# Kernel tuning notes

Hardware: AMD Instinct MI355X
Metric: run time of the kernel (lower is better)

## Reference

```python
import jax, jax.numpy as jnp
import numpy as np

N = 100000
E = 1600000
D = 128
BN_EPS = 1e-5


def setup_inputs() -> dict:
    key = jax.random.key(0)
    ks = jax.random.split(key, 12)
    s = 1.0 / np.sqrt(D)
    x = jax.random.normal(ks[0], (N, D), dtype=jnp.float32)
    edge_index = jax.random.randint(ks[1], (2, E), 0, N, dtype=jnp.int64)
    # Linear weights stored as [in, out] (i.e. torch W.T)
    w1a = jax.random.uniform(ks[2], (D, D), jnp.float32, -s, s)
    b1a = jax.random.uniform(ks[3], (D,), jnp.float32, -s, s)
    w1b = jax.random.uniform(ks[4], (D, D), jnp.float32, -s, s)
    b1b = jax.random.uniform(ks[5], (D,), jnp.float32, -s, s)
    gamma2 = jnp.ones((D,), jnp.float32)
    beta2 = jnp.zeros((D,), jnp.float32)
    w2a = jax.random.uniform(ks[6], (D, D), jnp.float32, -s, s)
    b2a = jax.random.uniform(ks[7], (D,), jnp.float32, -s, s)
    w2b = jax.random.uniform(ks[8], (D, D), jnp.float32, -s, s)
    b2b = jax.random.uniform(ks[9], (D,), jnp.float32, -s, s)
    return dict(x=x, edge_index=edge_index, w1a=w1a, b1a=b1a, w1b=w1b, b1b=b1b,
                gamma2=gamma2, beta2=beta2, w2a=w2a, b2a=b2a, w2b=w2b, b2b=b2b)


def _gin_conv(h, src, dst, wa, ba, wb, bb):
    # GINConv (eps=0): nn(sum_{j in N(i)} h_j + h_i), then 2-layer MLP
    agg = jax.ops.segment_sum(h[src], dst, num_segments=h.shape[0])
    z = agg + h
    z = jax.nn.relu(z @ wa + ba)
    return z @ wb + bb


def reference(x, edge_index, w1a, b1a, w1b, b1b, gamma2, beta2, w2a, b2a, w2b, b2b):
    src, dst = edge_index[0], edge_index[1]
    h = _gin_conv(x, src, dst, w1a, b1a, w1b, b1b)
    h = jax.nn.relu(h)
    # BatchNorm1d in training mode: batch mean / biased variance
    mean = jnp.mean(h, axis=0)
    var = jnp.mean((h - mean) ** 2, axis=0)
    h = (h - mean) * jax.lax.rsqrt(var + BN_EPS) * gamma2 + beta2
    return _gin_conv(h, src, dst, w2a, b2a, w2b, b2b)
```

## Files before the change

kernel.cpp:

```cpp
#include <hip/hip_runtime.h>

#define NNODES 100000
#define NEDGES 1600000
#define DIM 128
#define BN_EPS 1e-5f
#define NBUCK 1024
#define NB_USED ((NNODES + 127) / 128)

typedef unsigned int uint;
typedef unsigned short ushort_t;
using bhalf8  = __attribute__((ext_vector_type(8))) short;
using u16x8   = __attribute__((ext_vector_type(8))) unsigned short;
using f32x4_t = __attribute__((ext_vector_type(4))) float;

__device__ __forceinline__ float bf2f(uint u16) {
    return __uint_as_float(u16 << 16);
}
__device__ __forceinline__ uint pack2_bf16rn(float a, float b) {
    uint ua = __float_as_uint(a); ua += 0x7FFFu + ((ua >> 16) & 1u);
    uint ub = __float_as_uint(b); ub += 0x7FFFu + ((ub >> 16) & 1u);
    return __builtin_amdgcn_perm(ub, ua, 0x07060302u);
}

__device__ __forceinline__ int edge_src(const int* ei, int fl, int e) {
    return fl ? ei[2 * e] : ei[e];
}
__device__ __forceinline__ int edge_dst(const int* ei, int fl, int e) {
    return fl ? ei[2 * (NEDGES + e)] : ei[NEDGES + e];
}

__global__ __launch_bounds__(256) void k_setup(const int* __restrict__ ei,
                                               float* __restrict__ stats,
                                               int* __restrict__ flag,
                                               int* __restrict__ bcnt) {
    int t = threadIdx.x;
    stats[t] = 0.0f;
    ((int4*)bcnt)[t] = make_int4(0, 0, 0, 0);
    if (t == 0) {
        int orr = 0;
        for (int i = 1; i < 128; i += 2) orr |= ei[i];
        *flag = (orr == 0) ? 1 : 0;
    }
}

__global__ __launch_bounds__(256) void k_bcount(const int* __restrict__ ei,
                                                const int* __restrict__ flag,
                                                int* __restrict__ bcnt) {
    __shared__ int h[NBUCK];
    int t = threadIdx.x;
    for (int i = t; i < NBUCK; i += 256) h[i] = 0;
    __syncthreads();
    int fl = *flag;
    int per = (NEDGES + gridDim.x - 1) / gridDim.x;
    int e0 = blockIdx.x * per;
    int e1 = min(e0 + per, NEDGES);
    for (int e = e0 + t; e < e1; e += 256)
        atomicAdd(&h[edge_dst(ei, fl, e) >> 7], 1);
    __syncthreads();
    for (int i = t; i < NBUCK; i += 256)
        if (h[i]) atomicAdd(&bcnt[i], h[i]);
}

__global__ __launch_bounds__(256) void k_bscan(const int* __restrict__ bcnt,
                                               int* __restrict__ bstart,
                                               int* __restrict__ bcur) {
    __shared__ int wtot[4];
    int t = threadIdx.x, lane = t & 63, w = t >> 6;
    int4 v = ((const int4*)bcnt)[t];
    int s = v.x + v.y + v.z + v.w;
    int sc = s;
#pragma unroll
    for (int d = 1; d < 64; d <<= 1) {
        int n = __shfl_up(sc, d, 64);
        if (lane >= d) sc += n;
    }
    if (lane == 63) wtot[w] = sc;
    __syncthreads();
    int woff = 0;
    for (int i = 0; i < w; ++i) woff += wtot[i];
    int excl = woff + sc - s;
    int o0 = excl, o1 = o0 + v.x, o2 = o1 + v.y, o3 = o2 + v.z;
    bstart[t * 4]     = o0;  bcur[t * 4]     = o0;
    bstart[t * 4 + 1] = o1;  bcur[t * 4 + 1] = o1;
    bstart[t * 4 + 2] = o2;  bcur[t * 4 + 2] = o2;
    bstart[t * 4 + 3] = o3;  bcur[t * 4 + 3] = o3;
    if (t == 255) bstart[NBUCK] = o3 + v.w;
}

__global__ __launch_bounds__(256) void k_bpair(const int* __restrict__ ei,
                                               const int* __restrict__ flag,
                                               int* __restrict__ bcur,
                                               int* __restrict__ pairs) {
    __shared__ int h[NBUCK];
    __shared__ int base[NBUCK];
    int t = threadIdx.x;
    for (int i = t; i < NBUCK; i += 256) h[i] = 0;
    __syncthreads();
    int fl = *flag;
    int per = (NEDGES + gridDim.x - 1) / gridDim.x;
    int e0 = blockIdx.x * per;
    int e1 = min(e0 + per, NEDGES);
    for (int e = e0 + t; e < e1; e += 256)
        atomicAdd(&h[edge_dst(ei, fl, e) >> 7], 1);
    __syncthreads();
    for (int i = t; i < NBUCK; i += 256) {
        int c = h[i];
        base[i] = c ? atomicAdd(&bcur[i], c) : 0;
    }
    __syncthreads();
    for (int i = t; i < NBUCK; i += 256) h[i] = 0;
    __syncthreads();
    for (int e = e0 + t; e < e1; e += 256) {
        int s = edge_src(ei, fl, e);
        int d = edge_dst(ei, fl, e);
        int b = d >> 7;
        int pos = atomicAdd(&h[b], 1);
        pairs[base[b] + pos] = (s << 7) | (d & 127);
    }
}

__global__ __launch_bounds__(256) void k_bsort(const int* __restrict__ pairs,
                                               const int* __restrict__ bstart,
                                               int* __restrict__ C,
                                               int* __restrict__ ssrc) {
    __shared__ int cnt[128];
    __shared__ int off[128];
    int b = blockIdx.x;
    int t = threadIdx.x, lane = t & 63, w = t >> 6;
    int s = bstart[b], e = bstart[b + 1];
    if (t < 128) cnt[t] = 0;
    __syncthreads();
    for (int i = s + t; i < e; i += 256)
        atomicAdd(&cnt[pairs[i] & 127], 1);
    __syncthreads();
    if (w == 0) {
        int c0 = cnt[lane], c1 = cnt[64 + lane];
        int s0 = c0, s1 = c1;
#pragma unroll
        for (int d = 1; d < 64; d <<= 1) {
            int n0 = __shfl_up(s0, d, 64);
            int n1 = __shfl_up(s1, d, 64);
            if (lane >= d) { s0 += n0; s1 += n1; }
        }
        int tot0 = __shfl(s0, 63, 64);
        off[lane]      = s0 - c0;
        off[64 + lane] = tot0 + s1 - c1;
    }
    __syncthreads();
    if (t < 128) {
        int row = b * 128 + t;
        if (row < NNODES) C[row] = s + off[t] + cnt[t];
    }
    __syncthreads();
    for (int i = s + t; i < e; i += 256) {
        int p = pairs[i];
        int pos = atomicAdd(&off[p & 127], 1);
        ssrc[s + pos] = p >> 7;
    }
}

__global__ __launch_bounds__(256) void k_wprep(const float* __restrict__ w0,
                                               const float* __restrict__ w1,
                                               const float* __restrict__ w2,
                                               const float* __restrict__ w3,
                                               ushort_t* __restrict__ ob) {
    const float* w = (blockIdx.x == 0) ? w0 : (blockIdx.x == 1) ? w1
                   : (blockIdx.x == 2) ? w2 : w3;
    ushort_t* oh = ob + (size_t)blockIdx.x * 16384;
    for (int i = threadIdx.x; i < 16384; i += 256) {
        int k = i >> 7, n = i & 127;
        uint u = __float_as_uint(w[i]);
        u += 0x7FFFu + ((u >> 16) & 1u);
        oh[n * 128 + k] = (ushort_t)(u >> 16);
    }
}

__global__ __launch_bounds__(256) void k_xconv(const float* __restrict__ X,
                                               ushort_t* __restrict__ Xb) {
    size_t i = ((size_t)blockIdx.x * 256 + threadIdx.x) * 8;
    float4 a = *(const float4*)(X + i);
    float4 b = *(const float4*)(X + i + 4);
    union { uint4 q; u16x8 v; } o;
    o.q.x = pack2_bf16rn(a.x, a.y);
    o.q.y = pack2_bf16rn(a.z, a.w);
    o.q.z = pack2_bf16rn(b.x, b.y);
    o.q.w = pack2_bf16rn(b.z, b.w);
    *(u16x8*)(Xb + i) = o.v;
}

__device__ __forceinline__ void split8(const float4& f0, const float4& f1,
                                       bhalf8& h, bhalf8& l) {
    uint u[8] = { __float_as_uint(f0.x), __float_as_uint(f0.y),
                  __float_as_uint(f0.z), __float_as_uint(f0.w),
                  __float_as_uint(f1.x), __float_as_uint(f1.y),
                  __float_as_uint(f1.z), __float_as_uint(f1.w) };
    float fv[8] = { f0.x, f0.y, f0.z, f0.w, f1.x, f1.y, f1.z, f1.w };
    uint lu[8];
#pragma unroll
    for (int i = 0; i < 8; ++i) {
        float hf = __uint_as_float(u[i] & 0xffff0000u);
        lu[i] = __float_as_uint(fv[i] - hf);
    }
    union { uint4 q; bhalf8 s; } H, L;
    H.q.x = __builtin_amdgcn_perm(u[1], u[0], 0x07060302u);
    H.q.y = __builtin_amdgcn_perm(u[3], u[2], 0x07060302u);
    H.q.z = __builtin_amdgcn_perm(u[5], u[4], 0x07060302u);
    H.q.w = __builtin_amdgcn_perm(u[7], u[6], 0x07060302u);
    L.q.x = __builtin_amdgcn_perm(lu[1], lu[0], 0x07060302u);
    L.q.y = __builtin_amdgcn_perm(lu[3], lu[2], 0x07060302u);
    L.q.z = __builtin_amdgcn_perm(lu[5], lu[4], 0x07060302u);
    L.q.w = __builtin_amdgcn_perm(lu[7], lu[6], 0x07060302u);
    h = H.s; l = L.s;
}

template <bool BN, bool SELF_F32>
__global__ __launch_bounds__(256) void k_agg(const ushort_t* __restrict__ Xb,
                                             const float* __restrict__ Xf,
                                             float* __restrict__ Z,
                                             const int* __restrict__ ends,
                                             const int* __restrict__ ssrc,
                                             const float* __restrict__ scale,
                                             const float* __restrict__ shift) {
    int t = threadIdx.x;
    int g = t >> 4;
    int l = t & 15;
    int row = blockIdx.x * 16 + g;
    int c8 = l * 8;
    int start = (row == 0) ? 0 : ends[row - 1];
    int end = ends[row];

    float acc[8];
    if (SELF_F32) {
        float4 a0 = *(const float4*)(Xf + (size_t)row * DIM + c8);
        float4 a1 = *(const float4*)(Xf + (size_t)row * DIM + c8 + 4);
        acc[0] = a0.x; acc[1] = a0.y; acc[2] = a0.z; acc[3] = a0.w;
        acc[4] = a1.x; acc[5] = a1.y; acc[6] = a1.z; acc[7] = a1.w;
    } else {
        union { u16x8 v; uint u[4]; } sv;
        sv.v = *(const u16x8*)(Xb + (size_t)row * DIM + c8);
#pragma unroll
        for (int i = 0; i < 4; ++i) {
            acc[2 * i]     = bf2f(sv.u[i] << 16 >> 16);
            acc[2 * i + 1] = __uint_as_float(sv.u[i] & 0xffff0000u);
        }
    }

    int e = start;
    for (; e + 7 < end; e += 8) {
        union { u16x8 v; uint u[4]; } nv[8];
#pragma unroll
        for (int i = 0; i < 8; ++i) {
            int s0 = ssrc[e + i];
            nv[i].v = *(const u16x8*)(Xb + (size_t)s0 * DIM + c8);
        }
#pragma unroll
        for (int i = 0; i < 8; ++i) {
#pragma unroll
            for (int j = 0; j < 4; ++j) {
                acc[2 * j]     += bf2f(nv[i].u[j] & 0xffffu);
                acc[2 * j + 1] += __uint_as_float(nv[i].u[j] & 0xffff0000u);
            }
        }
    }
    for (; e < end; ++e) {
        int s0 = ssrc[e];
        union { u16x8 v; uint u[4]; } nv;
        nv.v = *(const u16x8*)(Xb + (size_t)s0 * DIM + c8);
#pragma unroll
        for (int j = 0; j < 4; ++j) {
            acc[2 * j]     += bf2f(nv.u[j] & 0xffffu);
            acc[2 * j + 1] += __uint_as_float(nv.u[j] & 0xffff0000u);
        }
    }

    if (BN) {
        float4 sc0 = *(const float4*)(scale + c8);
        float4 sc1 = *(const float4*)(scale + c8 + 4);
        float4 sh0 = *(const float4*)(shift + c8);
        float4 sh1 = *(const float4*)(shift + c8 + 4);
        float cnt = (float)(end - start + 1);
        acc[0] = fmaf(acc[0], sc0.x, cnt * sh0.x);
        acc[1] = fmaf(acc[1], sc0.y, cnt * sh0.y);
        acc[2] = fmaf(acc[2], sc0.z, cnt * sh0.z);
        acc[3] = fmaf(acc[3], sc0.w, cnt * sh0.w);
        acc[4] = fmaf(acc[4], sc1.x, cnt * sh1.x);
        acc[5] = fmaf(acc[5], sc1.y, cnt * sh1.y);
        acc[6] = fmaf(acc[6], sc1.z, cnt * sh1.z);
        acc[7] = fmaf(acc[7], sc1.w, cnt * sh1.w);
    }
    float* zp = Z + (size_t)row * DIM + c8;
    *(float4*)zp       = make_float4(acc[0], acc[1], acc[2], acc[3]);
    *(float4*)(zp + 4) = make_float4(acc[4], acc[5], acc[6], acc[7]);
}

__global__ void k_bn(float* stats, const float* __restrict__ gamma,
                     const float* __restrict__ beta) {
    int c = threadIdx.x;
    float s  = stats[c];
    float sq = stats[128 + c];
    float mean = s / (float)NNODES;
    float var  = sq / (float)NNODES - mean * mean;
    float sc = gamma[c] * rsqrtf(var + BN_EPS);
    float sh = beta[c] - mean * sc;
    stats[c]       = sc;
    stats[128 + c] = sh;
}

template <bool CONV1>
__global__ __launch_bounds__(256, 2) void k_mlp(const float* __restrict__ Z,
                                                const ushort_t* __restrict__ WAh,
                                                const ushort_t* __restrict__ WBh,
                                                const float* __restrict__ Ba,
                                                const float* __restrict__ Bb,
                                                float* __restrict__ OutF,
                                                ushort_t* __restrict__ OutB,
                                                float* __restrict__ stats) {
    __shared__ ushort_t wsl[16384];
    __shared__ float hbuf[64 * 128];
    __shared__ float lsum[128], lsq[128];
    char* hb = (char*)hbuf;

    int t = threadIdx.x;
    int w = t >> 6, l = t & 63;
    int lr = l & 15;
    int lg = l >> 4;
    int slane = (lr & 7) << 4;
    if (CONV1 && t < 128) { lsum[t] = 0.f; lsq[t] = 0.f; }

    int rowBase = blockIdx.x * 64 + w * 16;
    bool active = rowBase < NNODES;

#pragma unroll
    for (int i = 0; i < 8; ++i) {
        int c = i * 256 + t;
        uint4 v = ((const uint4*)WAh)[c];
        ((uint4*)wsl)[c ^ ((c >> 4) & 7)] = v;
    }
    int zrow = active ? (rowBase + lr) : 0;
    const float* zp = Z + (size_t)zrow * 128 + lg * 8;
    float4 zf[8];
#pragma unroll
    for (int ks = 0; ks < 4; ++ks) {
        zf[2 * ks]     = *(const float4*)(zp + ks * 32);
        zf[2 * ks + 1] = *(const float4*)(zp + ks * 32 + 4);
    }
    f32x4_t acc[8];
#pragma unroll
    for (int nt = 0; nt < 8; ++nt) {
        float b = Ba[nt * 16 + lr];
        acc[nt][0] = b; acc[nt][1] = b; acc[nt][2] = b; acc[nt][3] = b;
    }
    bhalf8 zh[4], zl[4];
#pragma unroll
    for (int ks = 0; ks < 4; ++ks) split8(zf[2 * ks], zf[2 * ks + 1], zh[ks], zl[ks]);
    __syncthreads();

#pragma unroll
    for (int ks = 0; ks < 4; ++ks) {
#pragma unroll
        for (int nt = 0; nt < 8; ++nt) {
            int waddr = ((nt * 16 + lr) << 8) + ((((ks << 6) + (lg << 4))) ^ slane);
            bhalf8 wh = *(const bhalf8*)((const char*)wsl + waddr);
            acc[nt] = __builtin_amdgcn_mfma_f32_16x16x32_bf16(zh[ks], wh, acc[nt], 0, 0, 0);
            acc[nt] = __builtin_amdgcn_mfma_f32_16x16x32_bf16(zl[ks], wh, acc[nt], 0, 0, 0);
        }
    }
#pragma unroll
    for (int nt = 0; nt < 8; ++nt) {
#pragma unroll
        for (int j = 0; j < 4; ++j) {
            int rl = w * 16 + lg * 4 + j;
            int boff = (rl * 512 + (nt * 16 + lr) * 4) ^ ((rl & 7) << 4);
            *(float*)(hb + boff) = fmaxf(acc[nt][j], 0.f);
        }
    }
    __syncthreads();

#pragma unroll
    for (int i = 0; i < 8; ++i) {
        int c = i * 256 + t;
        uint4 v = ((const uint4*)WBh)[c];
        ((uint4*)wsl)[c ^ ((c >> 4) & 7)] = v;
    }
    {
        int rl = w * 16 + lr;
        int swz = (rl & 7) << 4;
        int rbase = rl * 512 + lg * 32;
        float4 mf[8];
#pragma unroll
        for (int ks = 0; ks < 4; ++ks) {
            mf[2 * ks]     = *(const float4*)(hb + ((rbase + ks * 128) ^ swz));
            mf[2 * ks + 1] = *(const float4*)(hb + ((rbase + ks * 128 + 16) ^ swz));
        }
#pragma unroll
        for (int ks = 0; ks < 4; ++ks) split8(mf[2 * ks], mf[2 * ks + 1], zh[ks], zl[ks]);
    }
#pragma unroll
    for (int nt = 0; nt < 8; ++nt) {
        float b = Bb[nt * 16 + lr];
        acc[nt][0] = b; acc[nt][1] = b; acc[nt][2] = b; acc[nt][3] = b;
    }
    __syncthreads();

#pragma unroll
    for (int ks = 0; ks < 4; ++ks) {
#pragma unroll
        for (int nt = 0; nt < 8; ++nt) {
            int waddr = ((nt * 16 + lr) << 8) + ((((ks << 6) + (lg << 4))) ^ slane);
            bhalf8 wh = *(const bhalf8*)((const char*)wsl + waddr);
            acc[nt] = __builtin_amdgcn_mfma_f32_16x16x32_bf16(zh[ks], wh, acc[nt], 0, 0, 0);
            acc[nt] = __builtin_amdgcn_mfma_f32_16x16x32_bf16(zl[ks], wh, acc[nt], 0, 0, 0);
        }
    }

    if (CONV1 && active) {
#pragma unroll
        for (int nt = 0; nt < 8; ++nt) {
            float s = 0.f, q = 0.f;
#pragma unroll
            for (int j = 0; j < 4; ++j) {
                float v = fmaxf(acc[nt][j], 0.f);
                acc[nt][j] = v;
                s += v; q += v * v;
            }
            s += __shfl_xor(s, 16); s += __shfl_xor(s, 32);
            q += __shfl_xor(q, 16); q += __shfl_xor(q, 32);
            if (l < 16) {
                atomicAdd(&lsum[nt * 16 + l], s);
                atomicAdd(&lsq[nt * 16 + l], q);
            }
        }
    }
    __syncthreads();
#pragma unroll
    for (int nt = 0; nt < 8; ++nt) {
#pragma unroll
        for (int j = 0; j < 4; ++j) {
            int rl = w * 16 + lg * 4 + j;
            int boff = (rl * 512 + (nt * 16 + lr) * 4) ^ ((rl & 7) << 4);
            *(float*)(hb + boff) = acc[nt][j];
        }
    }
    if (CONV1) {
        __syncthreads();
        if (t < 128) {
            unsafeAtomicAdd(&stats[t], lsum[t]);
            unsafeAtomicAdd(&stats[128 + t], lsq[t]);
        }
    } else {
        __syncthreads();
    }
    {
        int r2 = t >> 2;
        int row = blockIdx.x * 64 + r2;
        if (row < NNODES) {
            int sw2 = (r2 & 7) << 4;
            int ch0 = (t & 3) * 8;
            if (CONV1) {
#pragma unroll
                for (int c = 0; c < 8; c += 2) {
                    float4 v0 = *(const float4*)(hb + ((r2 * 512 + (ch0 + c) * 16) ^ sw2));
                    float4 v1 = *(const float4*)(hb + ((r2 * 512 + (ch0 + c + 1) * 16) ^ sw2));
                    union { uint4 q; u16x8 v; } o;
                    o.q.x = pack2_bf16rn(v0.x, v0.y);
                    o.q.y = pack2_bf16rn(v0.z, v0.w);
                    o.q.z = pack2_bf16rn(v1.x, v1.y);
                    o.q.w = pack2_bf16rn(v1.z, v1.w);
                    *(u16x8*)(OutB + (size_t)row * 128 + (ch0 + c) * 4) = o.v;
                }
            } else {
#pragma unroll
                for (int c = 0; c < 8; ++c) {
                    float4 v = *(const float4*)(hb + ((r2 * 512 + (ch0 + c) * 16) ^ sw2));
                    *(float4*)(OutF + (size_t)row * 128 + (ch0 + c) * 4) = v;
                }
            }
        }
    }
}

extern "C" void kernel_launch(void* const* d_in, const int* in_sizes, int n_in,
                              void* d_out, int out_size, void* d_ws, size_t ws_size,
                              hipStream_t stream) {
    const float* x     = (const float*)d_in[0];
    const int*   ei    = (const int*)d_in[1];
    const float* w1a   = (const float*)d_in[2];
    const float* b1a   = (const float*)d_in[3];
    const float* w1b   = (const float*)d_in[4];
    const float* b1b   = (const float*)d_in[5];
    const float* gamma = (const float*)d_in[6];
    const float* beta  = (const float*)d_in[7];
    const float* w2a   = (const float*)d_in[8];
    const float* b2a   = (const float*)d_in[9];
    const float* w2b   = (const float*)d_in[10];
    const float* b2b   = (const float*)d_in[11];
    float* out = (float*)d_out;

    char*     ws     = (char*)d_ws;
    float*    stats  = (float*)ws;
    int*      flag   = (int*)(ws + 1024);
    int*      bcnt   = (int*)(ws + 4096);
    int*      bstart = (int*)(ws + 8192);
    int*      bcur   = (int*)(ws + 16384);
    int*      C      = (int*)(ws + 404096);
    int*      ssrc   = (int*)(ws + 804096);
    ushort_t* wbuf   = (ushort_t*)(ws + 0x700000);
    float*    zbuf   = (float*)(ws + 0x800000);
    int*      pairs  = (int*)(ws + 0x800000);

    ushort_t* xb  = (ushort_t*)d_out;
    ushort_t* hrb = (ushort_t*)d_out + (size_t)NNODES * DIM;

    const int aggBlocks = NNODES / 16;
    const int cvtBlocks = NNODES * DIM / (256 * 8);
    const int mlpBlocks = (NNODES + 63) / 64;

    k_setup<<<1, 256, 0, stream>>>(ei, stats, flag, bcnt);
    k_bcount<<<256, 256, 0, stream>>>(ei, flag, bcnt);
    k_bscan<<<1, 256, 0, stream>>>(bcnt, bstart, bcur);
    k_bpair<<<256, 256, 0, stream>>>(ei, flag, bcur, pairs);
    k_bsort<<<NB_USED, 256, 0, stream>>>(pairs, bstart, C, ssrc);
    k_wprep<<<4, 256, 0, stream>>>(w1a, w1b, w2a, w2b, wbuf);
    k_xconv<<<cvtBlocks, 256, 0, stream>>>(x, xb);
    k_agg<false, true><<<aggBlocks, 256, 0, stream>>>(xb, x, zbuf, C, ssrc, nullptr, nullptr);
    k_mlp<true><<<mlpBlocks, 256, 0, stream>>>(
        zbuf, wbuf, wbuf + 16384, b1a, b1b, nullptr, hrb, stats);
    k_bn<<<1, 128, 0, stream>>>(stats, gamma, beta);
    k_agg<true, false><<<aggBlocks, 256, 0, stream>>>(hrb, nullptr, zbuf, C, ssrc, stats, stats + DIM);
    k_mlp<false><<<mlpBlocks, 256, 0, stream>>>(
        zbuf, wbuf + 32768, wbuf + 49152, b2a, b2b, out, nullptr, nullptr);
}
```

Before: 317.1 us.

## Fuse neighbor aggregation into MLP kernel via shared-memory staging

After: 352.5 us. 1.11x slower.

```diff
diff --git a/kernel.cpp b/kernel.cpp
--- a/kernel.cpp
+++ b/kernel.cpp
@@ -213,86 +213,6 @@
     h = H.s; l = L.s;
 }
 
-template <bool BN, bool SELF_F32>
-__global__ __launch_bounds__(256) void k_agg(const ushort_t* __restrict__ Xb,
-                                             const float* __restrict__ Xf,
-                                             float* __restrict__ Z,
-                                             const int* __restrict__ ends,
-                                             const int* __restrict__ ssrc,
-                                             const float* __restrict__ scale,
-                                             const float* __restrict__ shift) {
-    int t = threadIdx.x;
-    int g = t >> 4;
-    int l = t & 15;
-    int row = blockIdx.x * 16 + g;
-    int c8 = l * 8;
-    int start = (row == 0) ? 0 : ends[row - 1];
-    int end = ends[row];
-
-    float acc[8];
-    if (SELF_F32) {
-        float4 a0 = *(const float4*)(Xf + (size_t)row * DIM + c8);
-        float4 a1 = *(const float4*)(Xf + (size_t)row * DIM + c8 + 4);
-        acc[0] = a0.x; acc[1] = a0.y; acc[2] = a0.z; acc[3] = a0.w;
-        acc[4] = a1.x; acc[5] = a1.y; acc[6] = a1.z; acc[7] = a1.w;
-    } else {
-        union { u16x8 v; uint u[4]; } sv;
-        sv.v = *(const u16x8*)(Xb + (size_t)row * DIM + c8);
-#pragma unroll
-        for (int i = 0; i < 4; ++i) {
-            acc[2 * i]     = bf2f(sv.u[i] << 16 >> 16);
-            acc[2 * i + 1] = __uint_as_float(sv.u[i] & 0xffff0000u);
-        }
-    }
-
-    int e = start;
-    for (; e + 7 < end; e += 8) {
-        union { u16x8 v; uint u[4]; } nv[8];
-#pragma unroll
-        for (int i = 0; i < 8; ++i) {
-            int s0 = ssrc[e + i];
-            nv[i].v = *(const u16x8*)(Xb + (size_t)s0 * DIM + c8);
-        }
-#pragma unroll
-        for (int i = 0; i < 8; ++i) {
-#pragma unroll
-            for (int j = 0; j < 4; ++j) {
-                acc[2 * j]     += bf2f(nv[i].u[j] & 0xffffu);
-                acc[2 * j + 1] += __uint_as_float(nv[i].u[j] & 0xffff0000u);
-            }
-        }
-    }
-    for (; e < end; ++e) {
-        int s0 = ssrc[e];
-        union { u16x8 v; uint u[4]; } nv;
-        nv.v = *(const u16x8*)(Xb + (size_t)s0 * DIM + c8);
-#pragma unroll
-        for (int j = 0; j < 4; ++j) {
-            acc[2 * j]     += bf2f(nv.u[j] & 0xffffu);
-            acc[2 * j + 1] += __uint_as_float(nv.u[j] & 0xffff0000u);
-        }
-    }
-
-    if (BN) {
-        float4 sc0 = *(const float4*)(scale + c8);
-        float4 sc1 = *(const float4*)(scale + c8 + 4);
-        float4 sh0 = *(const float4*)(shift + c8);
-        float4 sh1 = *(const float4*)(shift + c8 + 4);
-        float cnt = (float)(end - start + 1);
-        acc[0] = fmaf(acc[0], sc0.x, cnt * sh0.x);
-        acc[1] = fmaf(acc[1], sc0.y, cnt * sh0.y);
-        acc[2] = fmaf(acc[2], sc0.z, cnt * sh0.z);
-        acc[3] = fmaf(acc[3], sc0.w, cnt * sh0.w);
-        acc[4] = fmaf(acc[4], sc1.x, cnt * sh1.x);
-        acc[5] = fmaf(acc[5], sc1.y, cnt * sh1.y);
-        acc[6] = fmaf(acc[6], sc1.z, cnt * sh1.z);
-        acc[7] = fmaf(acc[7], sc1.w, cnt * sh1.w);
-    }
-    float* zp = Z + (size_t)row * DIM + c8;
-    *(float4*)zp       = make_float4(acc[0], acc[1], acc[2], acc[3]);
-    *(float4*)(zp + 4) = make_float4(acc[4], acc[5], acc[6], acc[7]);
-}
-
 __global__ void k_bn(float* stats, const float* __restrict__ gamma,
                      const float* __restrict__ beta) {
     int c = threadIdx.x;
@@ -307,42 +227,132 @@
 }
 
 template <bool CONV1>
-__global__ __launch_bounds__(256, 2) void k_mlp(const float* __restrict__ Z,
-                                                const ushort_t* __restrict__ WAh,
-                                                const ushort_t* __restrict__ WBh,
-                                                const float* __restrict__ Ba,
-                                                const float* __restrict__ Bb,
-                                                float* __restrict__ OutF,
-                                                ushort_t* __restrict__ OutB,
-                                                float* __restrict__ stats) {
+__global__ __launch_bounds__(256, 2) void k_conv(const ushort_t* __restrict__ Xb,
+                                                 const float* __restrict__ Xf,
+                                                 const int* __restrict__ ends,
+                                                 const int* __restrict__ ssrc,
+                                                 const ushort_t* __restrict__ WAh,
+                                                 const ushort_t* __restrict__ WBh,
+                                                 const float* __restrict__ Ba,
+                                                 const float* __restrict__ Bb,
+                                                 const float* __restrict__ scale,
+                                                 const float* __restrict__ shift,
+                                                 float* __restrict__ OutF,
+                                                 ushort_t* __restrict__ OutB,
+                                                 float* __restrict__ stats) {
     __shared__ ushort_t wsl[16384];
     __shared__ float hbuf[64 * 128];
     __shared__ float lsum[128], lsq[128];
     char* hb = (char*)hbuf;
 
     int t = threadIdx.x;
+
+#pragma unroll
+    for (int i = 0; i < 8; ++i) {
+        int c = i * 256 + t;
+        uint4 v = ((const uint4*)WAh)[c];
+        ((uint4*)wsl)[c ^ ((c >> 4) & 7)] = v;
+    }
+    if (CONV1 && t < 128) { lsum[t] = 0.f; lsq[t] = 0.f; }
+
+    {
+        int g = t >> 4, l16 = t & 15;
+        int c8 = l16 * 8;
+        float4 sc0, sc1, sh0, sh1;
+        if (!CONV1) {
+            sc0 = *(const float4*)(scale + c8);
+            sc1 = *(const float4*)(scale + c8 + 4);
+            sh0 = *(const float4*)(shift + c8);
+            sh1 = *(const float4*)(shift + c8 + 4);
+        }
+#pragma unroll
+        for (int i = 0; i < 4; ++i) {
+            int rl = g * 4 + i;
+            int row = blockIdx.x * 64 + rl;
+            float acc[8] = {0.f, 0.f, 0.f, 0.f, 0.f, 0.f, 0.f, 0.f};
+            if (row < NNODES) {
+                int start = (row == 0) ? 0 : ends[row - 1];
+                int end = ends[row];
+                if (CONV1) {
+                    float4 a0 = *(const float4*)(Xf + (size_t)row * DIM + c8);
+                    float4 a1 = *(const float4*)(Xf + (size_t)row * DIM + c8 + 4);
+                    acc[0] = a0.x; acc[1] = a0.y; acc[2] = a0.z; acc[3] = a0.w;
+                    acc[4] = a1.x; acc[5] = a1.y; acc[6] = a1.z; acc[7] = a1.w;
+                } else {
+                    union { u16x8 v; uint u[4]; } sv;
+                    sv.v = *(const u16x8*)(Xb + (size_t)row * DIM + c8);
+#pragma unroll
+                    for (int j = 0; j < 4; ++j) {
+                        acc[2 * j]     += bf2f(sv.u[j] & 0xffffu);
+                        acc[2 * j + 1] += __uint_as_float(sv.u[j] & 0xffff0000u);
+                    }
+                }
+                int e = start;
+                for (; e + 3 < end; e += 4) {
+                    union { u16x8 v; uint u[4]; } nv[4];
+#pragma unroll
+                    for (int k = 0; k < 4; ++k) {
+                        int s0 = ssrc[e + k];
+                        nv[k].v = *(const u16x8*)(Xb + (size_t)s0 * DIM + c8);
+                    }
+#pragma unroll
+                    for (int k = 0; k < 4; ++k) {
+#pragma unroll
+                        for (int j = 0; j < 4; ++j) {
+                            acc[2 * j]     += bf2f(nv[k].u[j] & 0xffffu);
+                            acc[2 * j + 1] += __uint_as_float(nv[k].u[j] & 0xffff0000u);
+                        }
+                    }
+                }
+                for (; e < end; ++e) {
+                    int s0 = ssrc[e];
+                    union { u16x8 v; uint u[4]; } nv;
+                    nv.v = *(const u16x8*)(Xb + (size_t)s0 * DIM + c8);
+#pragma unroll
+                    for (int j = 0; j < 4; ++j) {
+                        acc[2 * j]     += bf2f(nv.u[j] & 0xffffu);
+                        acc[2 * j + 1] += __uint_as_float(nv.u[j] & 0xffff0000u);
+                    }
+                }
+                if (!CONV1) {
+                    float cnt = (float)(end - start + 1);
+                    acc[0] = fmaf(acc[0], sc0.x, cnt * sh0.x);
+                    acc[1] = fmaf(acc[1], sc0.y, cnt * sh0.y);
+                    acc[2] = fmaf(acc[2], sc0.z, cnt * sh0.z);
+                    acc[3] = fmaf(acc[3], sc0.w, cnt * sh0.w);
+                    acc[4] = fmaf(acc[4], sc1.x, cnt * sh1.x);
+                    acc[5] = fmaf(acc[5], sc1.y, cnt * sh1.y);
+                    acc[6] = fmaf(acc[6], sc1.z, cnt * sh1.z);
+                    acc[7] = fmaf(acc[7], sc1.w, cnt * sh1.w);
+                }
+            }
+            int b0 = (rl * 512 + c8 * 4) ^ ((rl & 7) << 4);
+            int b1 = (rl * 512 + (c8 + 4) * 4) ^ ((rl & 7) << 4);
+            *(float4*)(hb + b0) = make_float4(acc[0], acc[1], acc[2], acc[3]);
+            *(float4*)(hb + b1) = make_float4(acc[4], acc[5], acc[6], acc[7]);
+        }
+    }
+    __syncthreads();
+
     int w = t >> 6, l = t & 63;
     int lr = l & 15;
     int lg = l >> 4;
     int slane = (lr & 7) << 4;
-    if (CONV1 && t < 128) { lsum[t] = 0.f; lsq[t] = 0.f; }
-
     int rowBase = blockIdx.x * 64 + w * 16;
     bool active = rowBase < NNODES;
 
-#pragma unroll
-    for (int i = 0; i < 8; ++i) {
-        int c = i * 256 + t;
-        uint4 v = ((const uint4*)WAh)[c];
-        ((uint4*)wsl)[c ^ ((c >> 4) & 7)] = v;
-    }
-    int zrow = active ? (rowBase + lr) : 0;
-    const float* zp = Z + (size_t)zrow * 128 + lg * 8;
-    float4 zf[8];
-#pragma unroll
-    for (int ks = 0; ks < 4; ++ks) {
-        zf[2 * ks]     = *(const float4*)(zp + ks * 32);
-        zf[2 * ks + 1] = *(const float4*)(zp + ks * 32 + 4);
+    bhalf8 zh[4], zl[4];
+    {
+        int rl = w * 16 + lr;
+        int swz = (rl & 7) << 4;
+        float4 zf[8];
+#pragma unroll
+        for (int ks = 0; ks < 4; ++ks) {
+            zf[2 * ks]     = *(const float4*)(hb + ((rl * 512 + (ks * 32 + lg * 8) * 4) ^ swz));
+            zf[2 * ks + 1] = *(const float4*)(hb + ((rl * 512 + (ks * 32 + lg * 8 + 4) * 4) ^ swz));
+        }
+#pragma unroll
+        for (int ks = 0; ks < 4; ++ks) split8(zf[2 * ks], zf[2 * ks + 1], zh[ks], zl[ks]);
     }
     f32x4_t acc[8];
 #pragma unroll
@@ -350,9 +360,6 @@
         float b = Ba[nt * 16 + lr];
         acc[nt][0] = b; acc[nt][1] = b; acc[nt][2] = b; acc[nt][3] = b;
     }
-    bhalf8 zh[4], zl[4];
-#pragma unroll
-    for (int ks = 0; ks < 4; ++ks) split8(zf[2 * ks], zf[2 * ks + 1], zh[ks], zl[ks]);
     __syncthreads();
 
 #pragma unroll
@@ -505,15 +512,13 @@
     int*      C      = (int*)(ws + 404096);
     int*      ssrc   = (int*)(ws + 804096);
     ushort_t* wbuf   = (ushort_t*)(ws + 0x700000);
-    float*    zbuf   = (float*)(ws + 0x800000);
     int*      pairs  = (int*)(ws + 0x800000);
+    ushort_t* hrb    = (ushort_t*)(ws + 0x1000000);
 
     ushort_t* xb  = (ushort_t*)d_out;
-    ushort_t* hrb = (ushort_t*)d_out + (size_t)NNODES * DIM;
-
-    const int aggBlocks = NNODES / 16;
-    const int cvtBlocks = NNODES * DIM / (256 * 8);
-    const int mlpBlocks = (NNODES + 63) / 64;
+
+    const int cvtBlocks  = NNODES * DIM / (256 * 8);
+    const int convBlocks = (NNODES + 63) / 64;
 
     k_setup<<<1, 256, 0, stream>>>(ei, stats, flag, bcnt);
     k_bcount<<<256, 256, 0, stream>>>(ei, flag, bcnt);
@@ -522,11 +527,11 @@
     k_bsort<<<NB_USED, 256, 0, stream>>>(pairs, bstart, C, ssrc);
     k_wprep<<<4, 256, 0, stream>>>(w1a, w1b, w2a, w2b, wbuf);
     k_xconv<<<cvtBlocks, 256, 0, stream>>>(x, xb);
-    k_agg<false, true><<<aggBlocks, 256, 0, stream>>>(xb, x, zbuf, C, ssrc, nullptr, nullptr);
-    k_mlp<true><<<mlpBlocks, 256, 0, stream>>>(
-        zbuf, wbuf, wbuf + 16384, b1a, b1b, nullptr, hrb, stats);
+    k_conv<true><<<convBlocks, 256, 0, stream>>>(
+        xb, x, C, ssrc, wbuf, wbuf + 16384, b1a, b1b, nullptr, nullptr,
+        nullptr, hrb, stats);
     k_bn<<<1, 128, 0, stream>>>(stats, gamma, beta);
-    k_agg<true, false><<<aggBlocks, 256, 0, stream>>>(hrb, nullptr, zbuf, C, ssrc, stats, stats + DIM);
-    k_mlp<false><<<mlpBlocks, 256, 0, stream>>>(
-        zbuf, wbuf + 32768, wbuf + 49152, b2a, b2b, out, nullptr, nullptr);
-}
+    k_conv<false><<<convBlocks, 256, 0, stream>>>(
+        hrb, nullptr, C, ssrc, wbuf + 32768, wbuf + 49152, b2a, b2b,
+        stats, stats + DIM, out, nullptr, nullptr);
+}
```

## Merge prep kernels, fold BN finalize into aggregation, sort edges by source within rows

Applied to the files above, without the earlier changes.

Measured after the change: 306.1 us. 1.04x faster.

```diff
diff --git a/kernel.cpp b/kernel.cpp
--- a/kernel.cpp
+++ b/kernel.cpp
@@ -29,17 +29,46 @@
     return fl ? ei[2 * (NEDGES + e)] : ei[NEDGES + e];
 }
 
-__global__ __launch_bounds__(256) void k_setup(const int* __restrict__ ei,
-                                               float* __restrict__ stats,
-                                               int* __restrict__ flag,
-                                               int* __restrict__ bcnt) {
+__global__ __launch_bounds__(256) void k_prep(const float* __restrict__ X,
+                                              const int* __restrict__ ei,
+                                              const float* __restrict__ w0,
+                                              const float* __restrict__ w1,
+                                              const float* __restrict__ w2,
+                                              const float* __restrict__ w3,
+                                              float* __restrict__ stats,
+                                              int* __restrict__ flag,
+                                              int* __restrict__ bcnt,
+                                              ushort_t* __restrict__ wbuf,
+                                              ushort_t* __restrict__ Xb) {
+    int bid = blockIdx.x;
     int t = threadIdx.x;
-    stats[t] = 0.0f;
-    ((int4*)bcnt)[t] = make_int4(0, 0, 0, 0);
-    if (t == 0) {
-        int orr = 0;
-        for (int i = 1; i < 128; i += 2) orr |= ei[i];
-        *flag = (orr == 0) ? 1 : 0;
+    if (bid < 4) {
+        const float* w = (bid == 0) ? w0 : (bid == 1) ? w1 : (bid == 2) ? w2 : w3;
+        ushort_t* oh = wbuf + (size_t)bid * 16384;
+        for (int i = t; i < 16384; i += 256) {
+            int k = i >> 7, n = i & 127;
+            uint u = __float_as_uint(w[i]);
+            u += 0x7FFFu + ((u >> 16) & 1u);
+            oh[n * 128 + k] = (ushort_t)(u >> 16);
+        }
+    } else if (bid == 4) {
+        stats[t] = 0.0f;
+        ((int4*)bcnt)[t] = make_int4(0, 0, 0, 0);
+        if (t == 0) {
+            int orr = 0;
+            for (int i = 1; i < 128; i += 2) orr |= ei[i];
+            *flag = (orr == 0) ? 1 : 0;
+        }
+    } else {
+        size_t i = ((size_t)(bid - 5) * 256 + t) * 8;
+        float4 a = *(const float4*)(X + i);
+        float4 b = *(const float4*)(X + i + 4);
+        union { uint4 q; u16x8 v; } o;
+        o.q.x = pack2_bf16rn(a.x, a.y);
+        o.q.y = pack2_bf16rn(a.z, a.w);
+        o.q.z = pack2_bf16rn(b.x, b.y);
+        o.q.w = pack2_bf16rn(b.z, b.w);
+        *(u16x8*)(Xb + i) = o.v;
     }
 }
 
@@ -123,69 +152,47 @@
                                                const int* __restrict__ bstart,
                                                int* __restrict__ C,
                                                int* __restrict__ ssrc) {
-    __shared__ int cnt[128];
-    __shared__ int off[128];
+    __shared__ int cnt[2048];
+    __shared__ int off[2048];
+    __shared__ int wtot[4];
     int b = blockIdx.x;
     int t = threadIdx.x, lane = t & 63, w = t >> 6;
     int s = bstart[b], e = bstart[b + 1];
-    if (t < 128) cnt[t] = 0;
-    __syncthreads();
-    for (int i = s + t; i < e; i += 256)
-        atomicAdd(&cnt[pairs[i] & 127], 1);
-    __syncthreads();
-    if (w == 0) {
-        int c0 = cnt[lane], c1 = cnt[64 + lane];
-        int s0 = c0, s1 = c1;
-#pragma unroll
-        for (int d = 1; d < 64; d <<= 1) {
-            int n0 = __shfl_up(s0, d, 64);
-            int n1 = __shfl_up(s1, d, 64);
-            if (lane >= d) { s0 += n0; s1 += n1; }
-        }
-        int tot0 = __shfl(s0, 63, 64);
-        off[lane]      = s0 - c0;
-        off[64 + lane] = tot0 + s1 - c1;
-    }
+    for (int i = t; i < 2048; i += 256) cnt[i] = 0;
+    __syncthreads();
+    for (int i = s + t; i < e; i += 256) {
+        int p = pairs[i];
+        atomicAdd(&cnt[(p & 127) * 16 + (p >> 20)], 1);
+    }
+    __syncthreads();
+    int base = t * 8, loc[8], sum = 0;
+#pragma unroll
+    for (int j = 0; j < 8; ++j) { loc[j] = cnt[base + j]; sum += loc[j]; }
+    int sc = sum;
+#pragma unroll
+    for (int d = 1; d < 64; d <<= 1) {
+        int n = __shfl_up(sc, d, 64);
+        if (lane >= d) sc += n;
+    }
+    if (lane == 63) wtot[w] = sc;
+    __syncthreads();
+    int woff = 0;
+    for (int i = 0; i < w; ++i) woff += wtot[i];
+    int run = woff + sc - sum;
+#pragma unroll
+    for (int j = 0; j < 8; ++j) { off[base + j] = run; run += loc[j]; }
     __syncthreads();
     if (t < 128) {
         int row = b * 128 + t;
-        if (row < NNODES) C[row] = s + off[t] + cnt[t];
+        if (row < NNODES) C[row] = s + off[t * 16 + 15] + cnt[t * 16 + 15];
     }
     __syncthreads();
     for (int i = s + t; i < e; i += 256) {
         int p = pairs[i];
-        int pos = atomicAdd(&off[p & 127], 1);
+        int k = (p & 127) * 16 + (p >> 20);
+        int pos = atomicAdd(&off[k], 1);
         ssrc[s + pos] = p >> 7;
     }
-}
-
-__global__ __launch_bounds__(256) void k_wprep(const float* __restrict__ w0,
-                                               const float* __restrict__ w1,
-                                               const float* __restrict__ w2,
-                                               const float* __restrict__ w3,
-                                               ushort_t* __restrict__ ob) {
-    const float* w = (blockIdx.x == 0) ? w0 : (blockIdx.x == 1) ? w1
-                   : (blockIdx.x == 2) ? w2 : w3;
-    ushort_t* oh = ob + (size_t)blockIdx.x * 16384;
-    for (int i = threadIdx.x; i < 16384; i += 256) {
-        int k = i >> 7, n = i & 127;
-        uint u = __float_as_uint(w[i]);
-        u += 0x7FFFu + ((u >> 16) & 1u);
-        oh[n * 128 + k] = (ushort_t)(u >> 16);
-    }
-}
-
-__global__ __launch_bounds__(256) void k_xconv(const float* __restrict__ X,
-                                               ushort_t* __restrict__ Xb) {
-    size_t i = ((size_t)blockIdx.x * 256 + threadIdx.x) * 8;
-    float4 a = *(const float4*)(X + i);
-    float4 b = *(const float4*)(X + i + 4);
-    union { uint4 q; u16x8 v; } o;
-    o.q.x = pack2_bf16rn(a.x, a.y);
-    o.q.y = pack2_bf16rn(a.z, a.w);
-    o.q.z = pack2_bf16rn(b.x, b.y);
-    o.q.w = pack2_bf16rn(b.z, b.w);
-    *(u16x8*)(Xb + i) = o.v;
 }
 
 __device__ __forceinline__ void split8(const float4& f0, const float4& f1,
@@ -219,9 +226,23 @@
                                              float* __restrict__ Z,
                                              const int* __restrict__ ends,
                                              const int* __restrict__ ssrc,
-                                             const float* __restrict__ scale,
-                                             const float* __restrict__ shift) {
+                                             const float* __restrict__ stats,
+                                             const float* __restrict__ gamma,
+                                             const float* __restrict__ beta) {
+    __shared__ float scs[128], shs[128];
     int t = threadIdx.x;
+    if (BN) {
+        if (t < 128) {
+            float s  = stats[t];
+            float sq = stats[128 + t];
+            float mean = s / (float)NNODES;
+            float var  = sq / (float)NNODES - mean * mean;
+            float sc = gamma[t] * rsqrtf(var + BN_EPS);
+            scs[t] = sc;
+            shs[t] = beta[t] - mean * sc;
+        }
+        __syncthreads();
+    }
     int g = t >> 4;
     int l = t & 15;
     int row = blockIdx.x * 16 + g;
@@ -240,7 +261,7 @@
         sv.v = *(const u16x8*)(Xb + (size_t)row * DIM + c8);
 #pragma unroll
         for (int i = 0; i < 4; ++i) {
-            acc[2 * i]     = bf2f(sv.u[i] << 16 >> 16);
+            acc[2 * i]     = bf2f(sv.u[i] & 0xffffu);
             acc[2 * i + 1] = __uint_as_float(sv.u[i] & 0xffff0000u);
         }
     }
@@ -274,10 +295,10 @@
     }
 
     if (BN) {
-        float4 sc0 = *(const float4*)(scale + c8);
-        float4 sc1 = *(const float4*)(scale + c8 + 4);
-        float4 sh0 = *(const float4*)(shift + c8);
-        float4 sh1 = *(const float4*)(shift + c8 + 4);
+        float4 sc0 = *(const float4*)(scs + c8);
+        float4 sc1 = *(const float4*)(scs + c8 + 4);
+        float4 sh0 = *(const float4*)(shs + c8);
+        float4 sh1 = *(const float4*)(shs + c8 + 4);
         float cnt = (float)(end - start + 1);
         acc[0] = fmaf(acc[0], sc0.x, cnt * sh0.x);
         acc[1] = fmaf(acc[1], sc0.y, cnt * sh0.y);
@@ -291,19 +312,6 @@
     float* zp = Z + (size_t)row * DIM + c8;
     *(float4*)zp       = make_float4(acc[0], acc[1], acc[2], acc[3]);
     *(float4*)(zp + 4) = make_float4(acc[4], acc[5], acc[6], acc[7]);
-}
-
-__global__ void k_bn(float* stats, const float* __restrict__ gamma,
-                     const float* __restrict__ beta) {
-    int c = threadIdx.x;
-    float s  = stats[c];
-    float sq = stats[128 + c];
-    float mean = s / (float)NNODES;
-    float var  = sq / (float)NNODES - mean * mean;
-    float sc = gamma[c] * rsqrtf(var + BN_EPS);
-    float sh = beta[c] - mean * sc;
-    stats[c]       = sc;
-    stats[128 + c] = sh;
 }
 
 template <bool CONV1>
@@ -511,22 +519,22 @@
     ushort_t* xb  = (ushort_t*)d_out;
     ushort_t* hrb = (ushort_t*)d_out + (size_t)NNODES * DIM;
 
-    const int aggBlocks = NNODES / 16;
-    const int cvtBlocks = NNODES * DIM / (256 * 8);
-    const int mlpBlocks = (NNODES + 63) / 64;
-
-    k_setup<<<1, 256, 0, stream>>>(ei, stats, flag, bcnt);
+    const int aggBlocks  = NNODES / 16;
+    const int prepBlocks = 5 + NNODES * DIM / (256 * 8);
+    const int mlpBlocks  = (NNODES + 63) / 64;
+
+    k_prep<<<prepBlocks, 256, 0, stream>>>(x, ei, w1a, w1b, w2a, w2b,
+                                           stats, flag, bcnt, wbuf, xb);
     k_bcount<<<256, 256, 0, stream>>>(ei, flag, bcnt);
     k_bscan<<<1, 256, 0, stream>>>(bcnt, bstart, bcur);
     k_bpair<<<256, 256, 0, stream>>>(ei, flag, bcur, pairs);
     k_bsort<<<NB_USED, 256, 0, stream>>>(pairs, bstart, C, ssrc);
-    k_wprep<<<4, 256, 0, stream>>>(w1a, w1b, w2a, w2b, wbuf);
-    k_xconv<<<cvtBlocks, 256, 0, stream>>>(x, xb);
-    k_agg<false, true><<<aggBlocks, 256, 0, stream>>>(xb, x, zbuf, C, ssrc, nullptr, nullptr);
+    k_agg<false, true><<<aggBlocks, 256, 0, stream>>>(xb, x, zbuf, C, ssrc,
+                                                      nullptr, nullptr, nullptr);
     k_mlp<true><<<mlpBlocks, 256, 0, stream>>>(
         zbuf, wbuf, wbuf + 16384, b1a, b1b, nullptr, hrb, stats);
-    k_bn<<<1, 128, 0, stream>>>(stats, gamma, beta);
-    k_agg<true, false><<<aggBlocks, 256, 0, stream>>>(hrb, nullptr, zbuf, C, ssrc, stats, stats + DIM);
+    k_agg<true, false><<<aggBlocks, 256, 0, stream>>>(hrb, nullptr, zbuf, C, ssrc,
+                                                      stats, gamma, beta);
     k_mlp<false><<<mlpBlocks, 256, 0, stream>>>(
         zbuf, wbuf + 32768, wbuf + 49152, b2a, b2b, out, nullptr, nullptr);
 }
```
